# Performance work log

Hardware: AMD Instinct MI355X
Metric: run time of the kernel (lower is better)

## Reference

```python
import jax, jax.numpy as jnp
import numpy as np

EPS_LOG = 2.220446049250313e-16  # np.finfo(float).eps used in ES_EE.ee
K = 2  # use_experts (top-k)


def _balance(v):
    v = v.astype(jnp.float32)
    # torch .var() is unbiased (ddof=1)
    return jnp.var(v, ddof=1) / (jnp.mean(v) ** 2 + 1e-10)


def setup_inputs() -> dict:
    key = jax.random.key(0)
    ks = jax.random.split(key, 8)
    B, C, H, W, E, D, HF = 2, 128, 128, 128, 6, 6, 512
    s = 0.02  # small init so exp(expert_out) stays in range
    return {
        "x": jax.random.normal(ks[0], (B, C, H, W), jnp.float32),
        "prompt": jax.random.normal(ks[1], (B, C), jnp.float32),
        "de_cls": jax.random.uniform(ks[2], (B, D), jnp.float32),
        "w_g": jax.random.normal(ks[3], (2 * C, E), jnp.float32) * s,
        "gate_boost": jnp.asarray(0.5, jnp.float32),
        "degra_w": jax.random.normal(ks[4], (D, E), jnp.float32) * s,
        "degra_b": jnp.zeros((E,), jnp.float32),
        "fc1_w": jax.random.normal(ks[5], (E, C, HF), jnp.float32) * s,
        "fc1_b": jnp.zeros((E, HF), jnp.float32),
        "fc2_w": jax.random.normal(ks[6], (E, HF, C), jnp.float32) * s,
        "fc2_b": jnp.zeros((E, C), jnp.float32),
    }


def reference(x, prompt, de_cls, w_g, gate_boost, degra_w, degra_b,
              fc1_w, fc1_b, fc2_w, fc2_b):
    # eval-mode forward (self.training == False -> no gating noise)
    B, C, H, W = x.shape
    N = B * H * W
    xf = jnp.transpose(x, (0, 2, 3, 1)).reshape(N, C)           # (b h w) c
    pf = jnp.broadcast_to(prompt[:, None, None, :], (B, H, W, C)).reshape(N, C)
    D = de_cls.shape[1]
    df = jnp.broadcast_to(de_cls[:, None, None, :], (B, H, W, D)).reshape(N, D)

    x_p = jnp.concatenate([xf, pf], axis=1)                     # [N, 2C]
    expert_bias = df @ degra_w + degra_b                        # degra_proj
    logits = x_p @ w_g + gate_boost * expert_bias               # [N, E]

    top_v, top_i = jax.lax.top_k(logits, K)
    gates_k = jax.nn.softmax(top_v, axis=1)                     # [N, K]
    w = jnp.zeros_like(logits).at[jnp.arange(N)[:, None], top_i].set(gates_k)

    Weight = w.sum(0)                                           # [E]
    s_load = (w > 0).sum(0).astype(jnp.float32)                 # w_load
    loss = _balance(Weight) + _balance(s_load)

    # per-expert Mlp on all tokens (w==0 rows contribute nothing to combine,
    # mathematically identical to the gather/scatter dispatch in ES_EE)
    hid = jax.nn.gelu(jnp.einsum('nc,ech->neh', xf, fc1_w) + fc1_b,
                      approximate=False)                        # [N, E, HF]
    out = jnp.einsum('neh,ehc->nec', hid, fc2_w) + fc2_b        # [N, E, C]

    # ES_EE.ee: log( sum_e gate_e * exp(out_e) ), zeros -> eps
    comb = jnp.einsum('ne,nec->nc', w, jnp.exp(out))
    comb = jnp.where(comb == 0, EPS_LOG, comb)
    y = jnp.log(comb)

    y = y.reshape(B, H, W, C).transpose(0, 3, 1, 2)             # b c h w
    return y, loss
```

## Files before the change

kernel.cpp:

```cpp
#include <hip/hip_runtime.h>
#include <math.h>

#define HW    16384
#define NTOK  32768
#define CDIM  128
#define HFDIM 512
#define NEXP  6

typedef __attribute__((ext_vector_type(8))) short short8;
typedef __attribute__((ext_vector_type(8))) unsigned short ushort8v;
typedef __attribute__((ext_vector_type(16))) float f32x16;
typedef unsigned long long u64;

#define OFF_XFB    0UL
#define OFF_LIST   8388608UL
#define OFF_GATES  9175040UL
#define OFF_OUTBUF 9437184UL
#define OFF_WT1    42991616UL
#define OFF_WT2    43778048UL
#define OFF_BIAS   44564480UL
#define OFF_CNT    44564736UL
#define OFF_WSUM   44564992UL

__device__ __forceinline__ unsigned int bf16_1(float f) {
    unsigned int u = __float_as_uint(f);
    return (u + 0x7FFFu + ((u >> 16) & 1)) >> 16;
}
__device__ __forceinline__ unsigned int bf16pair(float lo, float hi) {
    return bf16_1(lo) | (bf16_1(hi) << 16);
}
__device__ __forceinline__ float gelu_f(float v) {
    return __fdividef(v, 1.0f + __expf(-1.702f * v));
}
__device__ __forceinline__ short8 mk8(unsigned a, unsigned b, unsigned c, unsigned d) {
    union { unsigned u[4]; short8 s; } x;
    x.u[0] = a; x.u[1] = b; x.u[2] = c; x.u[3] = d;
    return x.s;
}
__device__ __forceinline__ short8 mkq(u64 lo, u64 hi) {
    union { u64 q[2]; short8 s; } x;
    x.q[0] = lo; x.q[1] = hi;
    return x.s;
}

#define GLDS16(src, dst) __builtin_amdgcn_global_load_lds( \
    (const __attribute__((address_space(1))) void*)(src),  \
    (__attribute__((address_space(3))) void*)(dst), 16, 0, 0)

__device__ __forceinline__ f32x16 MFMA_B(short8 a, short8 b, f32x16 c) {
    return __builtin_amdgcn_mfma_f32_32x32x16_bf16(a, b, c, 0, 0, 0);
}

__global__ __launch_bounds__(64) void prep_kernel(
    const float* __restrict__ prompt, const float* __restrict__ de_cls,
    const float* __restrict__ w_g, const float* __restrict__ gate_boost,
    const float* __restrict__ degra_w, const float* __restrict__ degra_b,
    float* __restrict__ bias, int* __restrict__ cnt, float* __restrict__ wsum)
{
    int t = threadIdx.x;
    if (t < 2 * NEXP) {
        int b = t / NEXP, e = t % NEXP;
        float acc = 0.f;
        for (int c = 0; c < CDIM; ++c)
            acc = fmaf(prompt[b*CDIM + c], w_g[(CDIM + c)*NEXP + e], acc);
        float db = 0.f;
        for (int d = 0; d < 6; ++d)
            db = fmaf(de_cls[b*6 + d], degra_w[d*NEXP + e], db);
        bias[b*NEXP + e] = acc + gate_boost[0] * (db + degra_b[e]);
    }
    if (t >= 32 && t < 32 + NEXP) cnt[t - 32] = 0;
    if (t >= 40 && t < 40 + NEXP) wsum[t - 40] = 0.f;
}

__global__ __launch_bounds__(256) void wconv_kernel(
    const float* __restrict__ fc1_w, const float* __restrict__ fc2_w,
    unsigned short* __restrict__ wt1, unsigned short* __restrict__ wt2)
{
    __shared__ unsigned short ls[128][128];
    const int bid = blockIdx.x;
    const int e = bid >> 3, which = (bid >> 2) & 1, ch = bid & 3;
    const int t = threadIdx.x;
    #pragma unroll 4
    for (int i = 0; i < 16; ++i) {
        int id = t + 256 * i;
        int k = id >> 5, q = id & 31;
        const float* p = which
            ? (fc2_w + (size_t)e*65536 + (size_t)(ch*128 + k)*128 + q*4)
            : (fc1_w + (size_t)e*65536 + (size_t)k*512 + ch*128 + q*4);
        float4 v = *(const float4*)p;
        u64 pk = (u64)bf16_1(v.x) | ((u64)bf16_1(v.y) << 16)
               | ((u64)bf16_1(v.z) << 32) | ((u64)bf16_1(v.w) << 48);
        *(u64*)&ls[k][q*4] = pk;
    }
    __syncthreads();
    #pragma unroll 2
    for (int i = 0; i < 8; ++i) {
        int id = t + 256 * i;
        int col = id & 127, kg = id >> 7;
        unsigned short v[8];
        #pragma unroll
        for (int j = 0; j < 8; ++j) v[j] = ls[kg*8 + j][col];
        u64 lo = (u64)v[0] | ((u64)v[1] << 16) | ((u64)v[2] << 32) | ((u64)v[3] << 48);
        u64 hi = (u64)v[4] | ((u64)v[5] << 16) | ((u64)v[6] << 32) | ((u64)v[7] << 48);
        if (which) {
            int h  = kg >> 3;
            int g0 = (kg & 7) * 2;
            unsigned short* d = wt2 + (size_t)e*65536 + (size_t)(ch*2 + h)*8192
                              + (size_t)col*64;
            *(u64*)(d + (((g0    ) ^ (col & 15)) << 2)) = lo;
            *(u64*)(d + (((g0 + 1) ^ (col & 15)) << 2)) = hi;
        } else {
            int4 pk;
            pk.x = (unsigned)(lo & 0xFFFFFFFFu); pk.y = (unsigned)(lo >> 32);
            pk.z = (unsigned)(hi & 0xFFFFFFFFu); pk.w = (unsigned)(hi >> 32);
            *(int4*)(wt1 + (((size_t)(e*4 + ch)) << 14)
                     + (size_t)col*128 + (((kg ^ (col & 15)) & 15) << 3)) = pk;
        }
    }
}

__global__ __launch_bounds__(256) void gate_kernel(
    const float* __restrict__ x, const float* __restrict__ w_g,
    const float* __restrict__ bias, unsigned short* __restrict__ xfb,
    int* __restrict__ list, float* __restrict__ gates,
    int* __restrict__ cnt, float* __restrict__ wsum)
{
    __shared__ float xs[CDIM][65];
    __shared__ float wgs[CDIM][NEXP];
    __shared__ int   cnt_s[NEXP];
    __shared__ float ws_s[NEXP];
    __shared__ int   base_s[NEXP];
    const int t = threadIdx.x;
    const int n0 = blockIdx.x * 64;
    const int b = n0 >> 14;
    const int hw0 = n0 & (HW - 1);

    for (int i = t; i < CDIM * NEXP; i += 256) wgs[i / NEXP][i % NEXP] = w_g[i];
    if (t < NEXP) { cnt_s[t] = 0; ws_s[t] = 0.f; }

    const float* xb = x + (size_t)b * CDIM * HW + hw0;
    #pragma unroll 4
    for (int i = 0; i < 32; ++i) {
        int idx = t + 256 * i;
        int c = idx >> 6, j = idx & 63;
        xs[c][j] = xb[(size_t)c * HW + j];
    }
    __syncthreads();
    unsigned int* xo = (unsigned int*)xfb;
    #pragma unroll 4
    for (int i = 0; i < 16; ++i) {
        int idx = t + 256 * i;
        int tk = idx >> 6, cp = idx & 63;
        xo[(size_t)(n0 + tk) * 64 + cp] = bf16pair(xs[2*cp][tk], xs[2*cp+1][tk]);
    }

    int i0 = 0, i1 = 0, s0 = 0, s1 = 0;
    float g0 = 0.f, g1 = 0.f;
    if (t < 64) {
        float lg[NEXP];
        #pragma unroll
        for (int e = 0; e < NEXP; ++e) lg[e] = bias[b*NEXP + e];
        for (int c = 0; c < CDIM; ++c) {
            float xv = xs[c][t];
            #pragma unroll
            for (int e = 0; e < NEXP; ++e) lg[e] = fmaf(xv, wgs[c][e], lg[e]);
        }
        i0 = 0;
        #pragma unroll
        for (int e = 1; e < NEXP; ++e) if (lg[e] > lg[i0]) i0 = e;
        i1 = (i0 == 0) ? 1 : 0;
        #pragma unroll
        for (int e = 0; e < NEXP; ++e) if (e != i0 && lg[e] > lg[i1]) i1 = e;
        float e1 = expf(lg[i1] - lg[i0]);
        g0 = 1.f / (1.f + e1);
        g1 = e1 * g0;
        s0 = atomicAdd(&cnt_s[i0], 1);
        s1 = atomicAdd(&cnt_s[i1], 1);
        atomicAdd(&ws_s[i0], g0);
        atomicAdd(&ws_s[i1], g1);
    }
    __syncthreads();
    if (t < NEXP) {
        base_s[t] = atomicAdd(&cnt[t], cnt_s[t]);
        atomicAdd(&wsum[t], ws_s[t]);
    }
    __syncthreads();
    if (t < 64) {
        int n = n0 + t;
        list[i0 * NTOK + base_s[i0] + s0] = 2 * n;
        list[i1 * NTOK + base_s[i1] + s1] = 2 * n + 1;
        gates[2 * n]     = g0;
        gates[2 * n + 1] = g1;
    }
}

__global__ void loss_kernel(const int* __restrict__ cnt,
                            const float* __restrict__ wsum,
                            float* __restrict__ out_loss)
{
    if (threadIdx.x == 0 && blockIdx.x == 0) {
        float mw = 0.f, mc = 0.f;
        for (int e = 0; e < NEXP; ++e) { mw += wsum[e]; mc += (float)cnt[e]; }
        mw /= NEXP; mc /= NEXP;
        float vw = 0.f, vc = 0.f;
        for (int e = 0; e < NEXP; ++e) {
            float dw = wsum[e] - mw, dc = (float)cnt[e] - mc;
            vw += dw * dw; vc += dc * dc;
        }
        vw /= (NEXP - 1); vc /= (NEXP - 1);
        out_loss[0] = vw / (mw * mw + 1e-10f) + vc / (mc * mc + 1e-10f);
    }
}

__global__ __launch_bounds__(128, 2) void expert_kernel(
    const unsigned short* __restrict__ xfb, const int* __restrict__ list,
    const int* __restrict__ cnt, const float* __restrict__ gates,
    const unsigned short* __restrict__ wt1, const unsigned short* __restrict__ wt2,
    const float* __restrict__ fc1_b, const float* __restrict__ fc2_b,
    unsigned short* __restrict__ outbuf)
{
    __shared__ unsigned short w1c[8192];
    __shared__ unsigned short w2c[8192];
    const int e = blockIdx.x;
    const int ne = cnt[e];
    const int base = blockIdx.y * 64;
    if (base >= ne) return;
    const int t = threadIdx.x;
    const int w = t >> 6, l = t & 63;
    const int l31 = l & 31, lh = l >> 5;
    const bool islo = (l < 32);

    int r = base + w*32 + l31;
    int a = (r < ne) ? list[e*NTOK + r] : -1;
    float g = (a >= 0) ? gates[a] : 0.f;
    int tok = (a >= 0) ? (a >> 1) : 0;

    short8 afr[8];
    {
        const unsigned short* xr = xfb + (size_t)tok*128 + lh*8;
        #pragma unroll
        for (int ks = 0; ks < 8; ++ks)
            afr[ks] = *(const short8*)(xr + ks*16);
    }

    f32x16 zz;
    #pragma unroll
    for (int i = 0; i < 16; ++i) zz[i] = 0.0f;
    f32x16 o0 = zz, o1 = zz, o2 = zz, o3 = zz;

    for (int gp = 0; gp < 8; ++gp) {
        {
            const unsigned short* s1 = wt1 + (((size_t)(e*4 + (gp >> 1))) << 14)
                                     + (gp & 1)*8192 + w*4096 + l*8;
            const unsigned short* s2 = wt2 + (size_t)e*65536 + (size_t)gp*8192
                                     + w*4096 + l*8;
            #pragma unroll
            for (int i = 0; i < 8; ++i)
                GLDS16(s1 + i*512, &w1c[w*4096 + i*512]);
            #pragma unroll
            for (int i = 0; i < 8; ++i)
                GLDS16(s2 + i*512, &w2c[w*4096 + i*512]);
        }
        __syncthreads();

        #pragma unroll
        for (int ch = 0; ch < 2; ++ch) {
            f32x16 c1 = zz;
            {
                int arow = ch*32 + l31;
                #pragma unroll
                for (int ks = 0; ks < 8; ++ks) {
                    int kk = ks*2 + lh;
                    short8 wf = *(const short8*)((const char*)w1c + arow*256
                                 + (((kk ^ (arow & 15)) & 15) << 4));
                    c1 = MFMA_B(wf, afr[ks], c1);
                }
            }
            const float* bb = fc1_b + (size_t)e*HFDIM + gp*64 + ch*32 + 4*lh;
            float4 b0 = *(const float4*)(bb);
            float4 b1 = *(const float4*)(bb + 8);
            float4 b2 = *(const float4*)(bb + 16);
            float4 b3 = *(const float4*)(bb + 24);
            float bias[16] = {b0.x, b0.y, b0.z, b0.w, b1.x, b1.y, b1.z, b1.w,
                              b2.x, b2.y, b2.z, b2.w, b3.x, b3.y, b3.z, b3.w};
            unsigned int pr[8];
            #pragma unroll
            for (int i = 0; i < 8; ++i) {
                pr[i] = bf16pair(gelu_f(c1[2*i]   + bias[2*i]),
                                 gelu_f(c1[2*i+1] + bias[2*i+1]));
            }
            unsigned int rx0 = __shfl_xor(islo ? pr[2] : pr[0], 32);
            unsigned int rx1 = __shfl_xor(islo ? pr[3] : pr[1], 32);
            unsigned int rx2 = __shfl_xor(islo ? pr[6] : pr[4], 32);
            unsigned int rx3 = __shfl_xor(islo ? pr[7] : pr[5], 32);
            short8 pa0 = mk8(islo ? pr[0] : rx0, islo ? pr[1] : rx1,
                             islo ? rx0 : pr[2], islo ? rx1 : pr[3]);
            short8 pa1 = mk8(islo ? pr[4] : rx2, islo ? pr[5] : rx3,
                             islo ? rx2 : pr[6], islo ? rx3 : pr[7]);

            #pragma unroll
            for (int ct = 0; ct < 4; ++ct) {
                int c = ct*32 + l31;
                const char* rb = (const char*)w2c + c*128;
                int xm = c & 15;
                int ga = ch*8 + lh*2;
                int gb = ch*8 + 4 + lh*2;
                u64 q0 = *(const u64*)(rb + (((ga    ) ^ xm) << 3));
                u64 q1 = *(const u64*)(rb + (((ga + 1) ^ xm) << 3));
                u64 q2 = *(const u64*)(rb + (((gb    ) ^ xm) << 3));
                u64 q3 = *(const u64*)(rb + (((gb + 1) ^ xm) << 3));
                short8 bf0 = mkq(q0, q1);
                short8 bf1 = mkq(q2, q3);
                if (ct == 0) { o0 = MFMA_B(pa0, bf0, o0); o0 = MFMA_B(pa1, bf1, o0); }
                else if (ct == 1) { o1 = MFMA_B(pa0, bf0, o1); o1 = MFMA_B(pa1, bf1, o1); }
                else if (ct == 2) { o2 = MFMA_B(pa0, bf0, o2); o2 = MFMA_B(pa1, bf1, o2); }
                else              { o3 = MFMA_B(pa0, bf0, o3); o3 = MFMA_B(pa1, bf1, o3); }
            }
        }
        __syncthreads();
    }

    float bc0 = fc2_b[(size_t)e*CDIM + l31];
    float bc1 = fc2_b[(size_t)e*CDIM + 32 + l31];
    float bc2 = fc2_b[(size_t)e*CDIM + 64 + l31];
    float bc3 = fc2_b[(size_t)e*CDIM + 96 + l31];
    #pragma unroll
    for (int rr = 0; rr < 16; ++rr) {
        int crow = (rr & 3) + 8*(rr >> 2) + 4*lh;
        int av   = __shfl(a, crow);
        float gv = __shfl(g, crow);
        if (av < 0) continue;
        unsigned short* po = outbuf + (size_t)av*CDIM + l31;
        po[0]  = (unsigned short)bf16_1(gv * __expf(o0[rr] + bc0));
        po[32] = (unsigned short)bf16_1(gv * __expf(o1[rr] + bc1));
        po[64] = (unsigned short)bf16_1(gv * __expf(o2[rr] + bc2));
        po[96] = (unsigned short)bf16_1(gv * __expf(o3[rr] + bc3));
    }
}

__global__ __launch_bounds__(256) void combine_kernel(
    const unsigned short* __restrict__ outbuf, float* __restrict__ out)
{
    __shared__ float ys[64][129];
    const int t = threadIdx.x;
    const int n0 = blockIdx.x * 64;
    const int b = n0 >> 14;
    const int hw0 = n0 & (HW - 1);
    #pragma unroll
    for (int i = 0; i < 4; ++i) {
        int idx = t + 256 * i;
        int tk = idx >> 4, c8 = (idx & 15) * 8;
        const unsigned short* p = outbuf + (size_t)(n0 + tk) * 256 + c8;
        ushort8v p0 = *(const ushort8v*)p;
        ushort8v p1 = *(const ushort8v*)(p + 128);
        const float EPSL = 2.2204460492503131e-16f;
        #pragma unroll
        for (int j = 0; j < 8; ++j) {
            float v = __uint_as_float((unsigned)p0[j] << 16)
                    + __uint_as_float((unsigned)p1[j] << 16);
            ys[tk][c8 + j] = __logf(v == 0.f ? EPSL : v);
        }
    }
    __syncthreads();
    float* ob = out + (size_t)b * CDIM * HW + hw0;
    #pragma unroll 4
    for (int i = 0; i < 32; ++i) {
        int idx = t + 256 * i;
        int c = idx >> 6;
        int j = idx & 63;
        ob[(size_t)c * HW + j] = ys[j][c];
    }
}

extern "C" void kernel_launch(void* const* d_in, const int* in_sizes, int n_in,
                              void* d_out, int out_size, void* d_ws, size_t ws_size,
                              hipStream_t stream)
{
    const float* x       = (const float*)d_in[0];
    const float* prompt  = (const float*)d_in[1];
    const float* de_cls  = (const float*)d_in[2];
    const float* w_g     = (const float*)d_in[3];
    const float* gboost  = (const float*)d_in[4];
    const float* degra_w = (const float*)d_in[5];
    const float* degra_b = (const float*)d_in[6];
    const float* fc1_w   = (const float*)d_in[7];
    const float* fc1_b   = (const float*)d_in[8];
    const float* fc2_w   = (const float*)d_in[9];
    const float* fc2_b   = (const float*)d_in[10];
    float* out = (float*)d_out;
    char* ws = (char*)d_ws;

    unsigned short* xfb  = (unsigned short*)(ws + OFF_XFB);
    int*   list   = (int*)(ws + OFF_LIST);
    float* gates  = (float*)(ws + OFF_GATES);
    unsigned short* outbuf = (unsigned short*)(ws + OFF_OUTBUF);
    unsigned short* wt1 = (unsigned short*)(ws + OFF_WT1);
    unsigned short* wt2 = (unsigned short*)(ws + OFF_WT2);
    float* bias   = (float*)(ws + OFF_BIAS);
    int*   cnt    = (int*)(ws + OFF_CNT);
    float* wsum   = (float*)(ws + OFF_WSUM);

    prep_kernel<<<1, 64, 0, stream>>>(prompt, de_cls, w_g, gboost, degra_w,
                                      degra_b, bias, cnt, wsum);
    wconv_kernel<<<48, 256, 0, stream>>>(fc1_w, fc2_w, wt1, wt2);
    gate_kernel<<<512, 256, 0, stream>>>(x, w_g, bias, xfb, list, gates, cnt, wsum);
    loss_kernel<<<1, 64, 0, stream>>>(cnt, wsum, out + (size_t)NTOK * CDIM);
    dim3 eg(NEXP, 512);
    expert_kernel<<<eg, 128, 0, stream>>>(xfb, list, cnt, gates, wt1, wt2,
                                          fc1_b, fc2_b, outbuf);
    combine_kernel<<<512, 256, 0, stream>>>(outbuf, out);
}
```

Measured before the change: 128.3 us.

## Double-buffer expert weight staging in LDS and widen blocks to 128 tokens

The expert kernel now runs 4 waves over 128 tokens per block instead of 2 waves over 64 tokens, so each staged weight chunk is reused by twice as many tokens. The LDS weight buffers are double-buffered: the next group's fc1/fc2 slices are issued asynchronously before computing on the current one, using a partial vmcnt wait plus a raw barrier in place of __syncthreads. The weight loads are split across waves (two load w1, two load w2). The aim is to hide global-to-LDS latency and cut redundant weight traffic, at the cost of twice the LDS per block (64KB), which may limit occupancy.

```diff
diff --git a/kernel.cpp b/kernel.cpp
--- a/kernel.cpp
+++ b/kernel.cpp
@@ -212,18 +212,18 @@
     }
 }
 
-__global__ __launch_bounds__(128, 2) void expert_kernel(
+__global__ __launch_bounds__(256, 2) void expert_kernel(
     const unsigned short* __restrict__ xfb, const int* __restrict__ list,
     const int* __restrict__ cnt, const float* __restrict__ gates,
     const unsigned short* __restrict__ wt1, const unsigned short* __restrict__ wt2,
     const float* __restrict__ fc1_b, const float* __restrict__ fc2_b,
     unsigned short* __restrict__ outbuf)
 {
-    __shared__ unsigned short w1c[8192];
-    __shared__ unsigned short w2c[8192];
+    __shared__ unsigned short w1c[2][8192];
+    __shared__ unsigned short w2c[2][8192];
     const int e = blockIdx.x;
     const int ne = cnt[e];
-    const int base = blockIdx.y * 64;
+    const int base = blockIdx.y * 128;
     if (base >= ne) return;
     const int t = threadIdx.x;
     const int w = t >> 6, l = t & 63;
@@ -243,25 +243,38 @@
             afr[ks] = *(const short8*)(xr + ks*16);
     }
 
+    auto STAGE = [&](int gp, int buf) {
+        if (w < 2) {
+            const unsigned short* s1 = wt1 + (((size_t)(e*4 + (gp >> 1))) << 14)
+                                     + (gp & 1)*8192 + w*4096 + l*8;
+            #pragma unroll
+            for (int i = 0; i < 8; ++i)
+                GLDS16(s1 + i*512, &w1c[buf][w*4096 + i*512]);
+        } else {
+            const unsigned short* s2 = wt2 + (size_t)e*65536 + (size_t)gp*8192
+                                     + (w - 2)*4096 + l*8;
+            #pragma unroll
+            for (int i = 0; i < 8; ++i)
+                GLDS16(s2 + i*512, &w2c[buf][(w - 2)*4096 + i*512]);
+        }
+    };
+
     f32x16 zz;
     #pragma unroll
     for (int i = 0; i < 16; ++i) zz[i] = 0.0f;
     f32x16 o0 = zz, o1 = zz, o2 = zz, o3 = zz;
 
+    STAGE(0, 0);
+
     for (int gp = 0; gp < 8; ++gp) {
-        {
-            const unsigned short* s1 = wt1 + (((size_t)(e*4 + (gp >> 1))) << 14)
-                                     + (gp & 1)*8192 + w*4096 + l*8;
-            const unsigned short* s2 = wt2 + (size_t)e*65536 + (size_t)gp*8192
-                                     + w*4096 + l*8;
-            #pragma unroll
-            for (int i = 0; i < 8; ++i)
-                GLDS16(s1 + i*512, &w1c[w*4096 + i*512]);
-            #pragma unroll
-            for (int i = 0; i < 8; ++i)
-                GLDS16(s2 + i*512, &w2c[w*4096 + i*512]);
-        }
-        __syncthreads();
+        const int cur = gp & 1;
+        if (gp < 7) {
+            STAGE(gp + 1, cur ^ 1);
+            asm volatile("s_waitcnt vmcnt(8)" ::: "memory");
+        } else {
+            asm volatile("s_waitcnt vmcnt(0)" ::: "memory");
+        }
+        __builtin_amdgcn_s_barrier();
 
         #pragma unroll
         for (int ch = 0; ch < 2; ++ch) {
@@ -271,7 +284,7 @@
                 #pragma unroll
                 for (int ks = 0; ks < 8; ++ks) {
                     int kk = ks*2 + lh;
-                    short8 wf = *(const short8*)((const char*)w1c + arow*256
+                    short8 wf = *(const short8*)((const char*)w1c[cur] + arow*256
                                  + (((kk ^ (arow & 15)) & 15) << 4));
                     c1 = MFMA_B(wf, afr[ks], c1);
                 }
@@ -301,7 +314,7 @@
             #pragma unroll
             for (int ct = 0; ct < 4; ++ct) {
                 int c = ct*32 + l31;
-                const char* rb = (const char*)w2c + c*128;
+                const char* rb = (const char*)w2c[cur] + c*128;
                 int xm = c & 15;
                 int ga = ch*8 + lh*2;
                 int gb = ch*8 + 4 + lh*2;
@@ -317,7 +330,7 @@
                 else              { o3 = MFMA_B(pa0, bf0, o3); o3 = MFMA_B(pa1, bf1, o3); }
             }
         }
-        __syncthreads();
+        __builtin_amdgcn_s_barrier();
     }
 
     float bc0 = fc2_b[(size_t)e*CDIM + l31];
@@ -405,8 +418,8 @@
     wconv_kernel<<<48, 256, 0, stream>>>(fc1_w, fc2_w, wt1, wt2);
     gate_kernel<<<512, 256, 0, stream>>>(x, w_g, bias, xfb, list, gates, cnt, wsum);
     loss_kernel<<<1, 64, 0, stream>>>(cnt, wsum, out + (size_t)NTOK * CDIM);
-    dim3 eg(NEXP, 512);
-    expert_kernel<<<eg, 128, 0, stream>>>(xfb, list, cnt, gates, wt1, wt2,
+    dim3 eg(NEXP, 256);
+    expert_kernel<<<eg, 256, 0, stream>>>(xfb, list, cnt, gates, wt1, wt2,
                                           fc1_b, fc2_b, outbuf);
     combine_kernel<<<512, 256, 0, stream>>>(outbuf, out);
 }
```

Measured after the change: 118.6 us. 7.6% less time.

## Split expert work over 4 waves with LDS hidden tile and staggered weight prefetch

Applied to the files above, without the earlier changes.

The expert kernel grows from 2 to 4 waves per block. Each wave pair now splits the hidden chunk and the output columns, so every wave keeps only two output accumulators instead of four. GELU activations go through a swizzled shared-memory tile instead of cross-lane shuffles. The fc1 and fc2 weight tiles are prefetched one step ahead with global-to-LDS loads, gated by manual vmcnt waits and raw barriers, so loads overlap with the MFMA work. The cost is extra LDS traffic and barriers per step, plus fragile hand-written waitcnt ordering.

```diff
diff --git a/kernel.cpp b/kernel.cpp
--- a/kernel.cpp
+++ b/kernel.cpp
@@ -31,11 +31,6 @@
 }
 __device__ __forceinline__ float gelu_f(float v) {
     return __fdividef(v, 1.0f + __expf(-1.702f * v));
-}
-__device__ __forceinline__ short8 mk8(unsigned a, unsigned b, unsigned c, unsigned d) {
-    union { unsigned u[4]; short8 s; } x;
-    x.u[0] = a; x.u[1] = b; x.u[2] = c; x.u[3] = d;
-    return x.s;
 }
 __device__ __forceinline__ short8 mkq(u64 lo, u64 hi) {
     union { u64 q[2]; short8 s; } x;
@@ -212,7 +207,7 @@
     }
 }
 
-__global__ __launch_bounds__(128, 2) void expert_kernel(
+__global__ __launch_bounds__(256, 4) void expert_kernel(
     const unsigned short* __restrict__ xfb, const int* __restrict__ list,
     const int* __restrict__ cnt, const float* __restrict__ gates,
     const unsigned short* __restrict__ wt1, const unsigned short* __restrict__ wt2,
@@ -221,6 +216,7 @@
 {
     __shared__ unsigned short w1c[8192];
     __shared__ unsigned short w2c[8192];
+    __shared__ unsigned short hsb[4096];
     const int e = blockIdx.x;
     const int ne = cnt[e];
     const int base = blockIdx.y * 64;
@@ -228,9 +224,10 @@
     const int t = threadIdx.x;
     const int w = t >> 6, l = t & 63;
     const int l31 = l & 31, lh = l >> 5;
-    const bool islo = (l < 32);
-
-    int r = base + w*32 + l31;
+    const int th = w & 1;
+    const int rh = w >> 1;
+
+    int r = base + th*32 + l31;
     int a = (r < ne) ? list[e*NTOK + r] : -1;
     float g = (a >= 0) ? gates[a] : 0.f;
     int tok = (a >= 0) ? (a >> 1) : 0;
@@ -246,95 +243,108 @@
     f32x16 zz;
     #pragma unroll
     for (int i = 0; i < 16; ++i) zz[i] = 0.0f;
-    f32x16 o0 = zz, o1 = zz, o2 = zz, o3 = zz;
+    f32x16 o0 = zz, o1 = zz;
+
+    auto STG1 = [&](int gp) {
+        const unsigned short* s1 = wt1 + (((size_t)(e*4 + (gp >> 1))) << 14)
+                                 + (gp & 1)*8192 + w*2048 + l*8;
+        #pragma unroll
+        for (int i = 0; i < 4; ++i)
+            GLDS16(s1 + i*512, &w1c[w*2048 + i*512]);
+    };
+    auto STG2 = [&](int gp) {
+        const unsigned short* s2 = wt2 + (size_t)e*65536 + (size_t)gp*8192
+                                 + w*2048 + l*8;
+        #pragma unroll
+        for (int i = 0; i < 4; ++i)
+            GLDS16(s2 + i*512, &w2c[w*2048 + i*512]);
+    };
+
+    STG1(0);
+    STG2(0);
+
+    const int tk = th*32 + l31;
+    const int xm = tk & 15;
 
     for (int gp = 0; gp < 8; ++gp) {
+        asm volatile("s_waitcnt vmcnt(4)" ::: "memory");
+        __builtin_amdgcn_s_barrier();
+
+        f32x16 c1 = zz;
         {
-            const unsigned short* s1 = wt1 + (((size_t)(e*4 + (gp >> 1))) << 14)
-                                     + (gp & 1)*8192 + w*4096 + l*8;
-            const unsigned short* s2 = wt2 + (size_t)e*65536 + (size_t)gp*8192
-                                     + w*4096 + l*8;
+            int arow = rh*32 + l31;
             #pragma unroll
-            for (int i = 0; i < 8; ++i)
-                GLDS16(s1 + i*512, &w1c[w*4096 + i*512]);
-            #pragma unroll
-            for (int i = 0; i < 8; ++i)
-                GLDS16(s2 + i*512, &w2c[w*4096 + i*512]);
-        }
-        __syncthreads();
-
-        #pragma unroll
-        for (int ch = 0; ch < 2; ++ch) {
-            f32x16 c1 = zz;
-            {
-                int arow = ch*32 + l31;
-                #pragma unroll
-                for (int ks = 0; ks < 8; ++ks) {
-                    int kk = ks*2 + lh;
-                    short8 wf = *(const short8*)((const char*)w1c + arow*256
-                                 + (((kk ^ (arow & 15)) & 15) << 4));
-                    c1 = MFMA_B(wf, afr[ks], c1);
-                }
+            for (int ks = 0; ks < 8; ++ks) {
+                int kk = ks*2 + lh;
+                short8 wf = *(const short8*)((const char*)w1c + arow*256
+                             + (((kk ^ (arow & 15)) & 15) << 4));
+                c1 = MFMA_B(wf, afr[ks], c1);
             }
-            const float* bb = fc1_b + (size_t)e*HFDIM + gp*64 + ch*32 + 4*lh;
+        }
+        {
+            const float* bb = fc1_b + (size_t)e*HFDIM + gp*64 + rh*32 + 4*lh;
             float4 b0 = *(const float4*)(bb);
             float4 b1 = *(const float4*)(bb + 8);
             float4 b2 = *(const float4*)(bb + 16);
             float4 b3 = *(const float4*)(bb + 24);
             float bias[16] = {b0.x, b0.y, b0.z, b0.w, b1.x, b1.y, b1.z, b1.w,
                               b2.x, b2.y, b2.z, b2.w, b3.x, b3.y, b3.z, b3.w};
-            unsigned int pr[8];
             #pragma unroll
             for (int i = 0; i < 8; ++i) {
-                pr[i] = bf16pair(gelu_f(c1[2*i]   + bias[2*i]),
-                                 gelu_f(c1[2*i+1] + bias[2*i+1]));
+                unsigned int pv = bf16pair(gelu_f(c1[2*i]   + bias[2*i]),
+                                           gelu_f(c1[2*i+1] + bias[2*i+1]));
+                int hf0 = rh*32 + 4*lh + (i & 1)*2 + (i >> 1)*8;
+                int gg  = hf0 >> 2;
+                *(unsigned int*)((char*)hsb + tk*128 + ((gg ^ xm) << 3)
+                                 + ((hf0 & 3) << 1)) = pv;
             }
-            unsigned int rx0 = __shfl_xor(islo ? pr[2] : pr[0], 32);
-            unsigned int rx1 = __shfl_xor(islo ? pr[3] : pr[1], 32);
-            unsigned int rx2 = __shfl_xor(islo ? pr[6] : pr[4], 32);
-            unsigned int rx3 = __shfl_xor(islo ? pr[7] : pr[5], 32);
-            short8 pa0 = mk8(islo ? pr[0] : rx0, islo ? pr[1] : rx1,
-                             islo ? rx0 : pr[2], islo ? rx1 : pr[3]);
-            short8 pa1 = mk8(islo ? pr[4] : rx2, islo ? pr[5] : rx3,
-                             islo ? rx2 : pr[6], islo ? rx3 : pr[7]);
-
+        }
+        asm volatile("s_waitcnt lgkmcnt(0)" ::: "memory");
+        __builtin_amdgcn_sched_barrier(0);
+        __builtin_amdgcn_s_barrier();
+
+        if (gp < 7) {
+            STG1(gp + 1);
+            asm volatile("s_waitcnt vmcnt(4)" ::: "memory");
+        } else {
+            asm volatile("s_waitcnt vmcnt(0)" ::: "memory");
+        }
+        __builtin_amdgcn_s_barrier();
+
+        #pragma unroll
+        for (int kg = 0; kg < 4; ++kg) {
+            int ga = kg*4 + lh*2;
+            const char* ra = (const char*)hsb + tk*128;
+            u64 a0 = *(const u64*)(ra + (((ga    ) ^ xm) << 3));
+            u64 a1 = *(const u64*)(ra + (((ga + 1) ^ xm) << 3));
+            short8 af2 = mkq(a0, a1);
             #pragma unroll
-            for (int ct = 0; ct < 4; ++ct) {
-                int c = ct*32 + l31;
+            for (int ct = 0; ct < 2; ++ct) {
+                int c = rh*64 + ct*32 + l31;
                 const char* rb = (const char*)w2c + c*128;
-                int xm = c & 15;
-                int ga = ch*8 + lh*2;
-                int gb = ch*8 + 4 + lh*2;
-                u64 q0 = *(const u64*)(rb + (((ga    ) ^ xm) << 3));
-                u64 q1 = *(const u64*)(rb + (((ga + 1) ^ xm) << 3));
-                u64 q2 = *(const u64*)(rb + (((gb    ) ^ xm) << 3));
-                u64 q3 = *(const u64*)(rb + (((gb + 1) ^ xm) << 3));
-                short8 bf0 = mkq(q0, q1);
-                short8 bf1 = mkq(q2, q3);
-                if (ct == 0) { o0 = MFMA_B(pa0, bf0, o0); o0 = MFMA_B(pa1, bf1, o0); }
-                else if (ct == 1) { o1 = MFMA_B(pa0, bf0, o1); o1 = MFMA_B(pa1, bf1, o1); }
-                else if (ct == 2) { o2 = MFMA_B(pa0, bf0, o2); o2 = MFMA_B(pa1, bf1, o2); }
-                else              { o3 = MFMA_B(pa0, bf0, o3); o3 = MFMA_B(pa1, bf1, o3); }
+                int xb = c & 15;
+                u64 q0 = *(const u64*)(rb + (((ga    ) ^ xb) << 3));
+                u64 q1 = *(const u64*)(rb + (((ga + 1) ^ xb) << 3));
+                short8 bf = mkq(q0, q1);
+                if (ct == 0) o0 = MFMA_B(af2, bf, o0);
+                else         o1 = MFMA_B(af2, bf, o1);
             }
         }
-        __syncthreads();
-    }
-
-    float bc0 = fc2_b[(size_t)e*CDIM + l31];
-    float bc1 = fc2_b[(size_t)e*CDIM + 32 + l31];
-    float bc2 = fc2_b[(size_t)e*CDIM + 64 + l31];
-    float bc3 = fc2_b[(size_t)e*CDIM + 96 + l31];
+        __builtin_amdgcn_s_barrier();
+        if (gp < 7) STG2(gp + 1);
+    }
+
+    float bc0 = fc2_b[(size_t)e*CDIM + rh*64 + l31];
+    float bc1 = fc2_b[(size_t)e*CDIM + rh*64 + 32 + l31];
     #pragma unroll
     for (int rr = 0; rr < 16; ++rr) {
         int crow = (rr & 3) + 8*(rr >> 2) + 4*lh;
         int av   = __shfl(a, crow);
         float gv = __shfl(g, crow);
         if (av < 0) continue;
-        unsigned short* po = outbuf + (size_t)av*CDIM + l31;
+        unsigned short* po = outbuf + (size_t)av*CDIM + rh*64 + l31;
         po[0]  = (unsigned short)bf16_1(gv * __expf(o0[rr] + bc0));
         po[32] = (unsigned short)bf16_1(gv * __expf(o1[rr] + bc1));
-        po[64] = (unsigned short)bf16_1(gv * __expf(o2[rr] + bc2));
-        po[96] = (unsigned short)bf16_1(gv * __expf(o3[rr] + bc3));
     }
 }
 
@@ -406,7 +416,7 @@
     gate_kernel<<<512, 256, 0, stream>>>(x, w_g, bias, xfb, list, gates, cnt, wsum);
     loss_kernel<<<1, 64, 0, stream>>>(cnt, wsum, out + (size_t)NTOK * CDIM);
     dim3 eg(NEXP, 512);
-    expert_kernel<<<eg, 128, 0, stream>>>(xfb, list, cnt, gates, wt1, wt2,
+    expert_kernel<<<eg, 256, 0, stream>>>(xfb, list, cnt, gates, wt1, wt2,
                                           fc1_b, fc2_b, outbuf);
     combine_kernel<<<512, 256, 0, stream>>>(outbuf, out);
 }
```

Result: faster. 112.8 us (-12.1%).
